# Performance work log

Hardware: AMD Instinct MI355X
Metric: run time of the kernel (lower is better)

Reference implementation:

```python
import jax, jax.numpy as jnp
import numpy as np

K = 60
BATCH, NCLS, H, W = 8, 2, 512, 512


def _neighbors(x):
    # x: [B,H,W] int32 in {0,1}. Returns P2..P9 clockwise starting north.
    p = jnp.pad(x, ((0, 0), (1, 1), (1, 1)))
    P2 = p[:, :-2, 1:-1]   # N
    P3 = p[:, :-2, 2:]     # NE
    P4 = p[:, 1:-1, 2:]    # E
    P5 = p[:, 2:, 2:]      # SE
    P6 = p[:, 2:, 1:-1]    # S
    P7 = p[:, 2:, :-2]     # SW
    P8 = p[:, 1:-1, :-2]   # W
    P9 = p[:, :-2, :-2]    # NW
    return P2, P3, P4, P5, P6, P7, P8, P9


def _substep(x, first):
    # One Zhang-Suen thinning sub-iteration (the algorithm used by
    # skimage.morphology.skeletonize for 2D images).
    P2, P3, P4, P5, P6, P7, P8, P9 = _neighbors(x)
    seq = (P2, P3, P4, P5, P6, P7, P8, P9, P2)
    # A = number of 0->1 transitions in circular neighbor sequence
    A = sum(((seq[i] == 0) & (seq[i + 1] == 1)).astype(jnp.int32) for i in range(8))
    Bn = P2 + P3 + P4 + P5 + P6 + P7 + P8 + P9
    if first:
        c3 = P2 * P4 * P6
        c4 = P4 * P6 * P8
    else:
        c3 = P2 * P4 * P8
        c4 = P2 * P6 * P8
    delete = (x == 1) & (Bn >= 2) & (Bn <= 6) & (A == 1) & (c3 == 0) & (c4 == 0)
    return x * (1 - delete.astype(x.dtype))


def _skeletonize(img):
    # img: [B,H,W] int32 binary. Iterate thinning until fixed point.
    def body(state):
        x, _ = state
        x2 = _substep(_substep(x, True), False)
        return x2, jnp.any(x2 != x)

    def cond(state):
        return state[1]

    out, _ = jax.lax.while_loop(cond, body, (img, jnp.array(True)))
    return out


def _conv(x, kernel, pad):
    # x: [B,1,H,W], kernel: [1,1,k,k], 'same' padding pad
    return jax.lax.conv_general_dilated(x, kernel, (1, 1), [(pad, pad), (pad, pad)])


def setup_inputs() -> dict:
    key = jax.random.key(0)
    k1, k2 = jax.random.split(key)
    pred = jax.random.normal(k1, (BATCH, NCLS, H, W), dtype=jnp.float32)
    target = jax.random.randint(k2, (BATCH, H, W), 0, NCLS, dtype=jnp.int32)
    return {"pred": pred, "target": target}


def reference(pred, target):
    # Per-pixel cross entropy, reduction='none'
    logp = jax.nn.log_softmax(pred, axis=1)
    L = -jnp.take_along_axis(logp, target[:, None].astype(jnp.int32), axis=1)[:, 0]  # [B,H,W]

    # Skeletonize the hard prediction (nonzero = foreground)
    A = jnp.argmax(pred, axis=1)
    skel = _skeletonize((A != 0).astype(jnp.int32))  # [B,H,W]
    Bm = skel[:, None].astype(pred.dtype)            # [B,1,H,W]

    # 3x3 neighbor count (center zeroed); endpoints C where product == 1
    k3 = jnp.ones((1, 1, 3, 3), pred.dtype).at[0, 0, 1, 1].set(0.0)
    C = Bm * _conv(Bm, k3, 1)
    C = (C == 1.0).astype(pred.dtype)

    # 9x9 endpoint density, scaled by K; zeros -> weight 1
    k9 = jnp.ones((1, 1, 9, 9), pred.dtype)
    N = _conv(C, k9, 4) * K
    Wmap = N + (N == 0.0).astype(pred.dtype)  # [B,1,H,W]

    return jnp.mean(Wmap[:, 0] * L)
```

## Files before the change

kernel.cpp:

```cpp
#include <hip/hip_runtime.h>

#define BATCH   8
#define HH      512
#define WW      512
#define IMGPIX  (HH * WW)
#define NPIX    (BATCH * IMGPIX)
#define NWORDS  (NPIX / 64)
#define WPR     8
#define FPSCALE 262144.0
#define MAXPAIR 256

typedef unsigned long long u64;
typedef unsigned int u32;

__global__ void prep_kernel(const float* __restrict__ pred, const int* __restrict__ target,
                            float* __restrict__ L, u64* __restrict__ xp,
                            u64* __restrict__ acc64, u32* __restrict__ ticket) {
    int i = blockIdx.x * blockDim.x + threadIdx.x;
    if (i == 0) { acc64[0] = 0ULL; ticket[0] = 0u; }
    if (i >= NPIX) return;
    int b = i >> 18;
    int hw = i & (IMGPIX - 1);
    float p0 = pred[((size_t)(2 * b) << 18) + hw];
    float p1 = pred[((size_t)(2 * b + 1) << 18) + hw];
    float ad = fabsf(p0 - p1);
    float lse = fmaxf(p0, p1) + __logf(1.0f + __expf(-ad));
    int t = target[i];
    L[i] = lse - (t ? p1 : p0);
    u64 word = __ballot(p1 > p0);
    if ((threadIdx.x & 63) == 0) xp[i >> 6] = word;
}

#define FA(a,b,c,s,cy) { u64 _x = (a)^(b); (s) = _x^(c); (cy) = ((a)&(b)) | ((c)&_x); }
#define HA(a,b,s,cy)   { (s) = (a)^(b); (cy) = (a)&(b); }

template<int FIRST>
__device__ __forceinline__ u64 zs_row(const u64* __restrict__ U, u64* __restrict__ M,
                                      const u64* __restrict__ D)
{
    u64 ch = 0;
    #pragma unroll
    for (int k = 0; k < WPR; ++k) {
        u64 Mc = M[k];
        if (Mc == 0ULL) continue;
        u64 Uc = U[k], Dc = D[k];
        u64 Up = k     ? U[k-1] : 0ULL;
        u64 Mp = k     ? M[k-1] : 0ULL;
        u64 Dp = k     ? D[k-1] : 0ULL;
        u64 Un = k < 7 ? U[k+1] : 0ULL;
        u64 Mn = k < 7 ? M[k+1] : 0ULL;
        u64 Dn = k < 7 ? D[k+1] : 0ULL;
        u64 P2 = Uc, P6 = Dc;
        u64 P3 = (Uc >> 1) | (Un << 63);
        u64 P4 = (Mc >> 1) | (Mn << 63);
        u64 P5 = (Dc >> 1) | (Dn << 63);
        u64 P9 = (Uc << 1) | (Up >> 63);
        u64 P8 = (Mc << 1) | (Mp >> 63);
        u64 P7 = (Dc << 1) | (Dp >> 63);

        u64 sa,ca, sb,cb, sc,cc, b0,cd, sd,ce, b1,cf, b2,b3;
        FA(P2,P3,P4, sa,ca);
        FA(P5,P6,P7, sb,cb);
        FA(P8,P9,sa, sc,cc);
        HA(sb,sc,    b0,cd);
        FA(ca,cb,cc, sd,ce);
        HA(sd,cd,    b1,cf);
        HA(ce,cf,    b2,b3);
        u64 ge2 = b1 | b2 | b3;
        u64 le6 = ~(b3 | (b0 & b1 & b2));

        u64 e, seen, two = 0;
        seen = (~P2) & P3;
        e = (~P3) & P4; two |= seen & e; seen |= e;
        e = (~P4) & P5; two |= seen & e; seen |= e;
        e = (~P5) & P6; two |= seen & e; seen |= e;
        e = (~P6) & P7; two |= seen & e; seen |= e;
        e = (~P7) & P8; two |= seen & e; seen |= e;
        e = (~P8) & P9; two |= seen & e; seen |= e;
        e = (~P9) & P2; two |= seen & e; seen |= e;
        u64 A1 = seen & ~two;

        u64 c34;
        if (FIRST) { u64 t = P4 & P6; c34 = t & (P2 | P8); }
        else       { u64 t = P2 & P8; c34 = t & (P4 | P6); }

        u64 del = Mc & ge2 & le6 & A1 & ~c34;
        M[k] = Mc ^ del;
        ch |= del;
    }
    return ch;
}

__device__ __forceinline__ int sidx(int h, int k) {
    return (h << 3) + (k ^ ((h >> 1) & 7));
}

__global__ __launch_bounds__(512)
void skel_kernel(const u64* __restrict__ xp, u64* __restrict__ eg)
{
    __shared__ u64 buf[2][HH * WPR];
    const int b = blockIdx.x;
    const int h = threadIdx.x;

    u64 M[WPR], U[WPR], D[WPR];
    const u64* src = xp + ((size_t)b << 12) + (size_t)h * WPR;
    #pragma unroll
    for (int k = 0; k < WPR; ++k) { M[k] = src[k]; buf[0][sidx(h, k)] = M[k]; }
    __syncthreads();

    const bool hasU = (h > 0), hasD = (h < HH - 1);

    for (int p = 0; p < MAXPAIR; ++p) {
        #pragma unroll
        for (int k = 0; k < WPR; ++k) {
            U[k] = hasU ? buf[0][sidx(h - 1, k)] : 0ULL;
            D[k] = hasD ? buf[0][sidx(h + 1, k)] : 0ULL;
        }
        u64 chA = zs_row<1>(U, M, D);
        #pragma unroll
        for (int k = 0; k < WPR; ++k) buf[1][sidx(h, k)] = M[k];
        __syncthreads();

        #pragma unroll
        for (int k = 0; k < WPR; ++k) {
            U[k] = hasU ? buf[1][sidx(h - 1, k)] : 0ULL;
            D[k] = hasD ? buf[1][sidx(h + 1, k)] : 0ULL;
        }
        u64 chB = zs_row<0>(U, M, D);
        #pragma unroll
        for (int k = 0; k < WPR; ++k) buf[0][sidx(h, k)] = M[k];
        if (!__syncthreads_or((chA | chB) != 0ULL)) break;
    }

    #pragma unroll
    for (int k = 0; k < WPR; ++k) {
        U[k] = hasU ? buf[0][sidx(h - 1, k)] : 0ULL;
        D[k] = hasD ? buf[0][sidx(h + 1, k)] : 0ULL;
    }
    u64* egr = eg + ((size_t)b << 12) + (size_t)h * WPR;
    #pragma unroll
    for (int k = 0; k < WPR; ++k) {
        u64 Mc = M[k];
        u64 Uc = U[k], Dc = D[k];
        u64 Up = k     ? U[k-1] : 0ULL;
        u64 Mp = k     ? M[k-1] : 0ULL;
        u64 Dp = k     ? D[k-1] : 0ULL;
        u64 Un = k < 7 ? U[k+1] : 0ULL;
        u64 Mn = k < 7 ? M[k+1] : 0ULL;
        u64 Dn = k < 7 ? D[k+1] : 0ULL;
        u64 P2 = Uc, P6 = Dc;
        u64 P3 = (Uc >> 1) | (Un << 63);
        u64 P4 = (Mc >> 1) | (Mn << 63);
        u64 P5 = (Dc >> 1) | (Dn << 63);
        u64 P9 = (Uc << 1) | (Up >> 63);
        u64 P8 = (Mc << 1) | (Mp >> 63);
        u64 P7 = (Dc << 1) | (Dp >> 63);
        u64 e, seen, two = 0;
        seen = P2;
        e = P3; two |= seen & e; seen |= e;
        e = P4; two |= seen & e; seen |= e;
        e = P5; two |= seen & e; seen |= e;
        e = P6; two |= seen & e; seen |= e;
        e = P7; two |= seen & e; seen |= e;
        e = P8; two |= seen & e; seen |= e;
        e = P9; two |= seen & e; seen |= e;
        egr[k] = Mc & seen & ~two;
    }
}

struct Planes { u64 p0, p1, p2, p3; };

__device__ __forceinline__ Planes vcount9(const u64 r[9]) {
    u64 s0,c0, s1,c1, s2,c2, p0,t0, t1,t2, p1,t3, p2,p3;
    FA(r[0],r[1],r[2], s0,c0);
    FA(r[3],r[4],r[5], s1,c1);
    FA(r[6],r[7],r[8], s2,c2);
    FA(s0,s1,s2, p0,t0);
    FA(c0,c1,c2, t1,t2);
    HA(t0,t1,    p1,t3);
    HA(t2,t3,    p2,p3);
    Planes P; P.p0 = p0; P.p1 = p1; P.p2 = p2; P.p3 = p3; return P;
}

__device__ __forceinline__ u64 spread8(u64 bb) {
    u64 s = (bb * 0x0101010101010101ULL) & 0x8040201008040201ULL;
    return ((s + 0x7f7f7f7f7f7f7f7fULL) >> 7) & 0x0101010101010101ULL;
}

__device__ __forceinline__ u64 vbytes(const Planes& P, int g) {
    int s = 8 * g;
    return  spread8((P.p0 >> s) & 0xFFULL)
         + (spread8((P.p1 >> s) & 0xFFULL) << 1)
         + (spread8((P.p2 >> s) & 0xFFULL) << 2)
         + (spread8((P.p3 >> s) & 0xFFULL) << 3);
}

__global__ __launch_bounds__(256)
void final_kernel(const float* __restrict__ L, const u64* __restrict__ eg,
                  u64* __restrict__ acc64, u32* __restrict__ ticket,
                  float* __restrict__ out) {
    __shared__ float sm[256];
    int wi = blockIdx.x * blockDim.x + threadIdx.x;
    int b  = wi >> 12;
    int h  = (wi >> 3) & (HH - 1);
    int wc = wi & 7;
    const u64* img = eg + ((size_t)b << 12);

    u64 rows[3][9];
    #pragma unroll
    for (int dh = -4; dh <= 4; ++dh) {
        int hh = h + dh;
        bool okh = (unsigned)hh < (unsigned)HH;
        const u64* rp = img + hh * WPR;
        rows[0][dh + 4] = (okh && wc > 0) ? rp[wc - 1] : 0ULL;
        rows[1][dh + 4] = okh             ? rp[wc]     : 0ULL;
        rows[2][dh + 4] = (okh && wc < 7) ? rp[wc + 1] : 0ULL;
    }
    Planes Pm = vcount9(rows[0]);
    Planes Pc = vcount9(rows[1]);
    Planes Pp = vcount9(rows[2]);

    u64 v[10];
    v[0] = vbytes(Pm, 7);
    #pragma unroll
    for (int g = 0; g < 8; ++g) v[g + 1] = vbytes(Pc, g);
    v[9] = vbytes(Pp, 0);

    const float4* Lr = (const float4*)(L + ((size_t)wi << 6));
    float acc = 0.0f;
    #pragma unroll
    for (int g = 0; g < 8; ++g) {
        u64 a = v[g + 1], lo = v[g], hi = v[g + 2];
        u64 n = a;
        #pragma unroll
        for (int d = 1; d <= 4; ++d) {
            n += (a >> (8 * d)) | (hi << (64 - 8 * d));
            n += (a << (8 * d)) | (lo >> (64 - 8 * d));
        }
        float4 f0 = Lr[2 * g], f1 = Lr[2 * g + 1];
        #pragma unroll
        for (int j = 0; j < 8; ++j) {
            int cnt = (int)((n >> (8 * j)) & 0xFFULL);
            float wgt = cnt ? (float)(60 * cnt) : 1.0f;
            float lv = (j < 4) ? ((j == 0) ? f0.x : (j == 1) ? f0.y : (j == 2) ? f0.z : f0.w)
                               : ((j == 4) ? f1.x : (j == 5) ? f1.y : (j == 6) ? f1.z : f1.w);
            acc += wgt * lv;
        }
    }

    sm[threadIdx.x] = acc;
    __syncthreads();
    for (int s = 128; s > 0; s >>= 1) {
        if (threadIdx.x < s) sm[threadIdx.x] += sm[threadIdx.x + s];
        __syncthreads();
    }
    if (threadIdx.x == 0) {
        u64 vfx = (u64)(long long)llrintf(sm[0] * (float)FPSCALE);
        atomicAdd(acc64, vfx);
        __threadfence();
        u32 t = atomicAdd(ticket, 1u);
        if (t == (u32)(gridDim.x - 1)) {
            __threadfence();
            u64 total = __hip_atomic_load(acc64, __ATOMIC_RELAXED, __HIP_MEMORY_SCOPE_AGENT);
            out[0] = (float)((double)(long long)total / (FPSCALE * (double)NPIX));
        }
    }
}

extern "C" void kernel_launch(void* const* d_in, const int* in_sizes, int n_in,
                              void* d_out, int out_size, void* d_ws, size_t ws_size,
                              hipStream_t stream) {
    const float* pred = (const float*)d_in[0];
    const int* target = (const int*)d_in[1];
    float* out = (float*)d_out;
    char* ws = (char*)d_ws;

    float* L    = (float*)(ws);
    u64* xp     = (u64*)(ws + 8388608);
    u64* eg     = (u64*)(ws + 8650752);
    u64* acc64  = (u64*)(ws + 8912896);
    u32* ticket = (u32*)(ws + 8912904);

    prep_kernel<<<dim3(NPIX / 256), dim3(256), 0, stream>>>(pred, target, L, xp, acc64, ticket);
    skel_kernel<<<dim3(BATCH), dim3(512), 0, stream>>>(xp, eg);
    final_kernel<<<dim3(NWORDS / 256), dim3(256), 0, stream>>>(L, eg, acc64, ticket, out);
}
```

Measured before the change: 59.45 us.

## Process two rows per thread in skeletonization kernel with 256 threads

```diff
diff --git a/kernel.cpp b/kernel.cpp
--- a/kernel.cpp
+++ b/kernel.cpp
@@ -35,13 +35,14 @@
 #define HA(a,b,s,cy)   { (s) = (a)^(b); (cy) = (a)&(b); }
 
 template<int FIRST>
-__device__ __forceinline__ u64 zs_row(const u64* __restrict__ U, u64* __restrict__ M,
-                                      const u64* __restrict__ D)
+__device__ __forceinline__ u64 zs_del(const u64* __restrict__ U, const u64* __restrict__ M,
+                                      const u64* __restrict__ D, u64* __restrict__ dels)
 {
     u64 ch = 0;
     #pragma unroll
     for (int k = 0; k < WPR; ++k) {
         u64 Mc = M[k];
+        dels[k] = 0ULL;
         if (Mc == 0ULL) continue;
         u64 Uc = U[k], Dc = D[k];
         u64 Up = k     ? U[k-1] : 0ULL;
@@ -85,7 +86,7 @@
         else       { u64 t = P2 & P8; c34 = t & (P4 | P6); }
 
         u64 del = Mc & ge2 & le6 & A1 & ~c34;
-        M[k] = Mc ^ del;
+        dels[k] = del;
         ch |= del;
     }
     return ch;
@@ -95,76 +96,92 @@
     return (h << 3) + (k ^ ((h >> 1) & 7));
 }
 
-__global__ __launch_bounds__(512)
+__global__ __launch_bounds__(256)
 void skel_kernel(const u64* __restrict__ xp, u64* __restrict__ eg)
 {
     __shared__ u64 buf[2][HH * WPR];
-    const int b = blockIdx.x;
-    const int h = threadIdx.x;
-
-    u64 M[WPR], U[WPR], D[WPR];
-    const u64* src = xp + ((size_t)b << 12) + (size_t)h * WPR;
-    #pragma unroll
-    for (int k = 0; k < WPR; ++k) { M[k] = src[k]; buf[0][sidx(h, k)] = M[k]; }
+    const int t  = threadIdx.x;
+    const int b  = blockIdx.x;
+    const int r0 = 2 * t, r1 = 2 * t + 1;
+
+    u64 M0[WPR], M1[WPR], U[WPR], D[WPR], d0[WPR], d1[WPR];
+    const u64* src = xp + ((size_t)b << 12) + (size_t)r0 * WPR;
+    #pragma unroll
+    for (int k = 0; k < WPR; ++k) {
+        M0[k] = src[k];        buf[0][sidx(r0, k)] = M0[k];
+        M1[k] = src[WPR + k];  buf[0][sidx(r1, k)] = M1[k];
+    }
     __syncthreads();
 
-    const bool hasU = (h > 0), hasD = (h < HH - 1);
+    const bool hasU = (r0 > 0), hasD = (r1 < HH - 1);
 
     for (int p = 0; p < MAXPAIR; ++p) {
         #pragma unroll
         for (int k = 0; k < WPR; ++k) {
-            U[k] = hasU ? buf[0][sidx(h - 1, k)] : 0ULL;
-            D[k] = hasD ? buf[0][sidx(h + 1, k)] : 0ULL;
-        }
-        u64 chA = zs_row<1>(U, M, D);
-        #pragma unroll
-        for (int k = 0; k < WPR; ++k) buf[1][sidx(h, k)] = M[k];
+            U[k] = hasU ? buf[0][sidx(r0 - 1, k)] : 0ULL;
+            D[k] = hasD ? buf[0][sidx(r1 + 1, k)] : 0ULL;
+        }
+        u64 chA = zs_del<1>(U, M0, M1, d0) | zs_del<1>(M0, M1, D, d1);
+        #pragma unroll
+        for (int k = 0; k < WPR; ++k) {
+            M0[k] ^= d0[k];  buf[1][sidx(r0, k)] = M0[k];
+            M1[k] ^= d1[k];  buf[1][sidx(r1, k)] = M1[k];
+        }
         __syncthreads();
 
         #pragma unroll
         for (int k = 0; k < WPR; ++k) {
-            U[k] = hasU ? buf[1][sidx(h - 1, k)] : 0ULL;
-            D[k] = hasD ? buf[1][sidx(h + 1, k)] : 0ULL;
-        }
-        u64 chB = zs_row<0>(U, M, D);
-        #pragma unroll
-        for (int k = 0; k < WPR; ++k) buf[0][sidx(h, k)] = M[k];
+            U[k] = hasU ? buf[1][sidx(r0 - 1, k)] : 0ULL;
+            D[k] = hasD ? buf[1][sidx(r1 + 1, k)] : 0ULL;
+        }
+        u64 chB = zs_del<0>(U, M0, M1, d0) | zs_del<0>(M0, M1, D, d1);
+        #pragma unroll
+        for (int k = 0; k < WPR; ++k) {
+            M0[k] ^= d0[k];  buf[0][sidx(r0, k)] = M0[k];
+            M1[k] ^= d1[k];  buf[0][sidx(r1, k)] = M1[k];
+        }
         if (!__syncthreads_or((chA | chB) != 0ULL)) break;
     }
 
     #pragma unroll
     for (int k = 0; k < WPR; ++k) {
-        U[k] = hasU ? buf[0][sidx(h - 1, k)] : 0ULL;
-        D[k] = hasD ? buf[0][sidx(h + 1, k)] : 0ULL;
-    }
-    u64* egr = eg + ((size_t)b << 12) + (size_t)h * WPR;
-    #pragma unroll
-    for (int k = 0; k < WPR; ++k) {
-        u64 Mc = M[k];
-        u64 Uc = U[k], Dc = D[k];
-        u64 Up = k     ? U[k-1] : 0ULL;
-        u64 Mp = k     ? M[k-1] : 0ULL;
-        u64 Dp = k     ? D[k-1] : 0ULL;
-        u64 Un = k < 7 ? U[k+1] : 0ULL;
-        u64 Mn = k < 7 ? M[k+1] : 0ULL;
-        u64 Dn = k < 7 ? D[k+1] : 0ULL;
-        u64 P2 = Uc, P6 = Dc;
-        u64 P3 = (Uc >> 1) | (Un << 63);
-        u64 P4 = (Mc >> 1) | (Mn << 63);
-        u64 P5 = (Dc >> 1) | (Dn << 63);
-        u64 P9 = (Uc << 1) | (Up >> 63);
-        u64 P8 = (Mc << 1) | (Mp >> 63);
-        u64 P7 = (Dc << 1) | (Dp >> 63);
-        u64 e, seen, two = 0;
-        seen = P2;
-        e = P3; two |= seen & e; seen |= e;
-        e = P4; two |= seen & e; seen |= e;
-        e = P5; two |= seen & e; seen |= e;
-        e = P6; two |= seen & e; seen |= e;
-        e = P7; two |= seen & e; seen |= e;
-        e = P8; two |= seen & e; seen |= e;
-        e = P9; two |= seen & e; seen |= e;
-        egr[k] = Mc & seen & ~two;
+        U[k] = hasU ? buf[0][sidx(r0 - 1, k)] : 0ULL;
+        D[k] = hasD ? buf[0][sidx(r1 + 1, k)] : 0ULL;
+    }
+    u64* egr = eg + ((size_t)b << 12) + (size_t)r0 * WPR;
+    #pragma unroll
+    for (int half = 0; half < 2; ++half) {
+        const u64* Ur = half ? M0 : U;
+        const u64* Mr = half ? M1 : M0;
+        const u64* Dr = half ? D  : M1;
+        #pragma unroll
+        for (int k = 0; k < WPR; ++k) {
+            u64 Mc = Mr[k];
+            u64 Uc = Ur[k], Dc = Dr[k];
+            u64 Up = k     ? Ur[k-1] : 0ULL;
+            u64 Mp = k     ? Mr[k-1] : 0ULL;
+            u64 Dp = k     ? Dr[k-1] : 0ULL;
+            u64 Un = k < 7 ? Ur[k+1] : 0ULL;
+            u64 Mn = k < 7 ? Mr[k+1] : 0ULL;
+            u64 Dn = k < 7 ? Dr[k+1] : 0ULL;
+            u64 P2 = Uc, P6 = Dc;
+            u64 P3 = (Uc >> 1) | (Un << 63);
+            u64 P4 = (Mc >> 1) | (Mn << 63);
+            u64 P5 = (Dc >> 1) | (Dn << 63);
+            u64 P9 = (Uc << 1) | (Up >> 63);
+            u64 P8 = (Mc << 1) | (Mp >> 63);
+            u64 P7 = (Dc << 1) | (Dp >> 63);
+            u64 e, seen, two = 0;
+            seen = P2;
+            e = P3; two |= seen & e; seen |= e;
+            e = P4; two |= seen & e; seen |= e;
+            e = P5; two |= seen & e; seen |= e;
+            e = P6; two |= seen & e; seen |= e;
+            e = P7; two |= seen & e; seen |= e;
+            e = P8; two |= seen & e; seen |= e;
+            e = P9; two |= seen & e; seen |= e;
+            egr[half * WPR + k] = Mc & seen & ~two;
+        }
     }
 }
 
@@ -282,6 +299,6 @@
     u32* ticket = (u32*)(ws + 8912904);
 
     prep_kernel<<<dim3(NPIX / 256), dim3(256), 0, stream>>>(pred, target, L, xp, acc64, ticket);
-    skel_kernel<<<dim3(BATCH), dim3(512), 0, stream>>>(xp, eg);
+    skel_kernel<<<dim3(BATCH), dim3(256), 0, stream>>>(xp, eg);
     final_kernel<<<dim3(NWORDS / 256), dim3(256), 0, stream>>>(L, eg, acc64, ticket, out);
 }
```

After: 61.75 us. 3.9% more time.

## Split each skeleton row across two threads with halo words

Applied to the files above, without the earlier changes.

```diff
diff --git a/kernel.cpp b/kernel.cpp
--- a/kernel.cpp
+++ b/kernel.cpp
@@ -34,22 +34,41 @@
 #define FA(a,b,c,s,cy) { u64 _x = (a)^(b); (s) = _x^(c); (cy) = ((a)&(b)) | ((c)&_x); }
 #define HA(a,b,s,cy)   { (s) = (a)^(b); (cy) = (a)&(b); }
 
+__device__ __forceinline__ int sidx(int h, int k) {
+    return (h << 3) + (k ^ ((h >> 1) & 7));
+}
+
+__device__ __forceinline__ void load6(const u64* __restrict__ B, int h, int s, bool hasRow,
+                                      u64* __restrict__ A) {
+    if (!hasRow) {
+        #pragma unroll
+        for (int j = 0; j < 6; ++j) A[j] = 0ULL;
+        return;
+    }
+    if (s == 0) {
+        A[0] = 0ULL;
+        #pragma unroll
+        for (int j = 0; j < 5; ++j) A[j + 1] = B[sidx(h, j)];
+    } else {
+        #pragma unroll
+        for (int j = 0; j < 5; ++j) A[j] = B[sidx(h, 3 + j)];
+        A[5] = 0ULL;
+    }
+}
+
 template<int FIRST>
-__device__ __forceinline__ u64 zs_row(const u64* __restrict__ U, u64* __restrict__ M,
-                                      const u64* __restrict__ D)
+__device__ __forceinline__ u64 zs_del4(const u64* __restrict__ Uw, const u64* __restrict__ Mw,
+                                       const u64* __restrict__ Dw, u64* __restrict__ dels)
 {
     u64 ch = 0;
     #pragma unroll
-    for (int k = 0; k < WPR; ++k) {
-        u64 Mc = M[k];
+    for (int k = 0; k < 4; ++k) {
+        u64 Mc = Mw[k + 1];
+        dels[k] = 0ULL;
         if (Mc == 0ULL) continue;
-        u64 Uc = U[k], Dc = D[k];
-        u64 Up = k     ? U[k-1] : 0ULL;
-        u64 Mp = k     ? M[k-1] : 0ULL;
-        u64 Dp = k     ? D[k-1] : 0ULL;
-        u64 Un = k < 7 ? U[k+1] : 0ULL;
-        u64 Mn = k < 7 ? M[k+1] : 0ULL;
-        u64 Dn = k < 7 ? D[k+1] : 0ULL;
+        u64 Uc = Uw[k + 1], Dc = Dw[k + 1];
+        u64 Up = Uw[k],     Mp = Mw[k],     Dp = Dw[k];
+        u64 Un = Uw[k + 2], Mn = Mw[k + 2], Dn = Dw[k + 2];
         u64 P2 = Uc, P6 = Dc;
         u64 P3 = (Uc >> 1) | (Un << 63);
         u64 P4 = (Mc >> 1) | (Mn << 63);
@@ -85,69 +104,70 @@
         else       { u64 t = P2 & P8; c34 = t & (P4 | P6); }
 
         u64 del = Mc & ge2 & le6 & A1 & ~c34;
-        M[k] = Mc ^ del;
+        dels[k] = del;
         ch |= del;
     }
     return ch;
 }
 
-__device__ __forceinline__ int sidx(int h, int k) {
-    return (h << 3) + (k ^ ((h >> 1) & 7));
-}
-
-__global__ __launch_bounds__(512)
+__global__ __launch_bounds__(1024)
 void skel_kernel(const u64* __restrict__ xp, u64* __restrict__ eg)
 {
     __shared__ u64 buf[2][HH * WPR];
-    const int b = blockIdx.x;
-    const int h = threadIdx.x;
-
-    u64 M[WPR], U[WPR], D[WPR];
-    const u64* src = xp + ((size_t)b << 12) + (size_t)h * WPR;
-    #pragma unroll
-    for (int k = 0; k < WPR; ++k) { M[k] = src[k]; buf[0][sidx(h, k)] = M[k]; }
+    const int t  = threadIdx.x;
+    const int b  = blockIdx.x;
+    const int h  = t & (HH - 1);
+    const int s  = t >> 9;
+    const int w0 = s << 2;
+
+    u64 Mw[6], Uw[6], Dw[6], d[4];
+    const u64* src = xp + ((size_t)b << 12) + (size_t)h * WPR + w0;
+    #pragma unroll
+    for (int k = 0; k < 4; ++k) {
+        Mw[k + 1] = src[k];
+        buf[0][sidx(h, w0 + k)] = Mw[k + 1];
+    }
     __syncthreads();
 
     const bool hasU = (h > 0), hasD = (h < HH - 1);
 
     for (int p = 0; p < MAXPAIR; ++p) {
-        #pragma unroll
-        for (int k = 0; k < WPR; ++k) {
-            U[k] = hasU ? buf[0][sidx(h - 1, k)] : 0ULL;
-            D[k] = hasD ? buf[0][sidx(h + 1, k)] : 0ULL;
-        }
-        u64 chA = zs_row<1>(U, M, D);
-        #pragma unroll
-        for (int k = 0; k < WPR; ++k) buf[1][sidx(h, k)] = M[k];
+        load6(buf[0], h - 1, s, hasU, Uw);
+        load6(buf[0], h + 1, s, hasD, Dw);
+        Mw[0] = s ? buf[0][sidx(h, 3)] : 0ULL;
+        Mw[5] = s ? 0ULL : buf[0][sidx(h, 4)];
+        u64 chA = zs_del4<1>(Uw, Mw, Dw, d);
+        #pragma unroll
+        for (int k = 0; k < 4; ++k) {
+            Mw[k + 1] ^= d[k];
+            buf[1][sidx(h, w0 + k)] = Mw[k + 1];
+        }
         __syncthreads();
 
-        #pragma unroll
-        for (int k = 0; k < WPR; ++k) {
-            U[k] = hasU ? buf[1][sidx(h - 1, k)] : 0ULL;
-            D[k] = hasD ? buf[1][sidx(h + 1, k)] : 0ULL;
-        }
-        u64 chB = zs_row<0>(U, M, D);
-        #pragma unroll
-        for (int k = 0; k < WPR; ++k) buf[0][sidx(h, k)] = M[k];
+        load6(buf[1], h - 1, s, hasU, Uw);
+        load6(buf[1], h + 1, s, hasD, Dw);
+        Mw[0] = s ? buf[1][sidx(h, 3)] : 0ULL;
+        Mw[5] = s ? 0ULL : buf[1][sidx(h, 4)];
+        u64 chB = zs_del4<0>(Uw, Mw, Dw, d);
+        #pragma unroll
+        for (int k = 0; k < 4; ++k) {
+            Mw[k + 1] ^= d[k];
+            buf[0][sidx(h, w0 + k)] = Mw[k + 1];
+        }
         if (!__syncthreads_or((chA | chB) != 0ULL)) break;
     }
 
-    #pragma unroll
-    for (int k = 0; k < WPR; ++k) {
-        U[k] = hasU ? buf[0][sidx(h - 1, k)] : 0ULL;
-        D[k] = hasD ? buf[0][sidx(h + 1, k)] : 0ULL;
-    }
-    u64* egr = eg + ((size_t)b << 12) + (size_t)h * WPR;
-    #pragma unroll
-    for (int k = 0; k < WPR; ++k) {
-        u64 Mc = M[k];
-        u64 Uc = U[k], Dc = D[k];
-        u64 Up = k     ? U[k-1] : 0ULL;
-        u64 Mp = k     ? M[k-1] : 0ULL;
-        u64 Dp = k     ? D[k-1] : 0ULL;
-        u64 Un = k < 7 ? U[k+1] : 0ULL;
-        u64 Mn = k < 7 ? M[k+1] : 0ULL;
-        u64 Dn = k < 7 ? D[k+1] : 0ULL;
+    load6(buf[0], h - 1, s, hasU, Uw);
+    load6(buf[0], h + 1, s, hasD, Dw);
+    Mw[0] = s ? buf[0][sidx(h, 3)] : 0ULL;
+    Mw[5] = s ? 0ULL : buf[0][sidx(h, 4)];
+    u64* egr = eg + ((size_t)b << 12) + (size_t)h * WPR + w0;
+    #pragma unroll
+    for (int k = 0; k < 4; ++k) {
+        u64 Mc = Mw[k + 1];
+        u64 Uc = Uw[k + 1], Dc = Dw[k + 1];
+        u64 Up = Uw[k],     Mp = Mw[k],     Dp = Dw[k];
+        u64 Un = Uw[k + 2], Mn = Mw[k + 2], Dn = Dw[k + 2];
         u64 P2 = Uc, P6 = Dc;
         u64 P3 = (Uc >> 1) | (Un << 63);
         u64 P4 = (Mc >> 1) | (Mn << 63);
@@ -282,6 +302,6 @@
     u32* ticket = (u32*)(ws + 8912904);
 
     prep_kernel<<<dim3(NPIX / 256), dim3(256), 0, stream>>>(pred, target, L, xp, acc64, ticket);
-    skel_kernel<<<dim3(BATCH), dim3(512), 0, stream>>>(xp, eg);
+    skel_kernel<<<dim3(BATCH), dim3(1024), 0, stream>>>(xp, eg);
     final_kernel<<<dim3(NWORDS / 256), dim3(256), 0, stream>>>(L, eg, acc64, ticket, out);
 }
```

Result: no change. 58.56 us (-1.5%).
